# Optimization experiments

Measured on AMD Instinct MI355X. Metric: run time of the kernel, lower is better.

Reference implementation:

```python
import jax, jax.numpy as jnp
import numpy as np

EPS = 1e-5
HEADS = 8
DIM_HEAD = 64
SCALE = DIM_HEAD ** -0.5
DEPTH = 4


def _layernorm(x, g, b):
    mu = jnp.mean(x, axis=-1, keepdims=True)
    var = jnp.var(x, axis=-1, keepdims=True)
    return (x - mu) * jax.lax.rsqrt(var + EPS) * g + b


def setup_inputs() -> dict:
    key = jax.random.key(0)
    ks = jax.random.split(key, 8)
    b, n, dim, mlp = 4, 1024, 512, 2048
    inner = HEADS * DIM_HEAD
    D = DEPTH
    s = 0.02  # realistic init scale
    return {
        "x": jax.random.normal(ks[0], (b, n, dim), jnp.float32),
        "ln1_g": jnp.ones((D, dim), jnp.float32),
        "ln1_b": jnp.zeros((D, dim), jnp.float32),
        "w_qkv": jax.random.normal(ks[1], (D, dim, 3 * inner), jnp.float32) * s,
        "reattn_w": jax.random.normal(ks[2], (D, HEADS, HEADS), jnp.float32),
        "rln_g": jnp.ones((D, HEADS), jnp.float32),
        "rln_b": jnp.zeros((D, HEADS), jnp.float32),
        "w_out": jax.random.normal(ks[3], (D, inner, dim), jnp.float32) * s,
        "b_out": jnp.zeros((D, dim), jnp.float32),
        "ln2_g": jnp.ones((D, dim), jnp.float32),
        "ln2_b": jnp.zeros((D, dim), jnp.float32),
        "w1": jax.random.normal(ks[4], (D, dim, mlp), jnp.float32) * s,
        "b1": jnp.zeros((D, mlp), jnp.float32),
        "w2": jax.random.normal(ks[5], (D, mlp, dim), jnp.float32) * s,
        "b2": jnp.zeros((D, dim), jnp.float32),
    }


def _attention(x, ln_g, ln_b, w_qkv, rw, rg, rb, w_out, b_out):
    b, n, dim = x.shape
    h, d = HEADS, DIM_HEAD
    hn = _layernorm(x, ln_g, ln_b)
    qkv = hn @ w_qkv  # [b, n, 3*h*d]
    q, k, v = jnp.split(qkv, 3, axis=-1)
    def to_heads(t):
        return t.reshape(b, n, h, d).transpose(0, 2, 1, 3)  # b h n d
    q, k, v = to_heads(q), to_heads(k), to_heads(v)
    dots = jnp.einsum('bhid,bhjd->bhij', q, k) * SCALE
    attn = jax.nn.softmax(dots, axis=-1)
    # cross-head re-attention mix
    attn = jnp.einsum('bhij,hg->bgij', attn, rw)
    # LayerNorm over the head axis (axis=1)
    mu = jnp.mean(attn, axis=1, keepdims=True)
    var = jnp.var(attn, axis=1, keepdims=True)
    attn = (attn - mu) * jax.lax.rsqrt(var + EPS)
    attn = attn * rg[None, :, None, None] + rb[None, :, None, None]
    out = jnp.einsum('bhij,bhjd->bhid', attn, v)
    out = out.transpose(0, 2, 1, 3).reshape(b, n, h * d)
    return out @ w_out + b_out


def _ffn(x, ln_g, ln_b, w1, b1, w2, b2):
    hn = _layernorm(x, ln_g, ln_b)
    hid = jax.nn.gelu(hn @ w1 + b1, approximate=False)
    return hid @ w2 + b2


def reference(x, ln1_g, ln1_b, w_qkv, reattn_w, rln_g, rln_b, w_out, b_out,
              ln2_g, ln2_b, w1, b1, w2, b2):
    for l in range(DEPTH):
        x = x + _attention(x, ln1_g[l], ln1_b[l], w_qkv[l], reattn_w[l],
                           rln_g[l], rln_b[l], w_out[l], b_out[l])
        x = x + _ffn(x, ln2_g[l], ln2_b[l], w1[l], b1[l], w2[l], b2[l])
        x = jnp.tanh(x)
    return x
```

## Files before the change

kernel.cpp:

```cpp
#include <hip/hip_runtime.h>
#include <math.h>

#define B 4
#define N 1024
#define DM 512
#define H 8
#define MLP 2048
#define TOK (B * N)
#define QKVW (3 * DM)
#define EPS 1e-5f
#define SCALE 0.125f

#define PS_HN  ((long)TOK * DM)
#define PS_WQ  ((long)QKVW * DM)
#define PS_VT  ((long)B * H * 64 * N)

using short8 = __attribute__((ext_vector_type(8))) short;
using f32x4  = __attribute__((ext_vector_type(4))) float;
using u32x4  = __attribute__((ext_vector_type(4))) unsigned int;

__device__ __forceinline__ ushort f2b(float v) {
    unsigned int u = __builtin_bit_cast(unsigned int, v);
    u += 0x7fff + ((u >> 16) & 1);
    return (ushort)(u >> 16);
}
__device__ __forceinline__ float b2f(ushort u) {
    return __builtin_bit_cast(float, (unsigned int)u << 16);
}
__device__ __forceinline__ void split3(float v, ushort& h, ushort& l, ushort& q2) {
    h = f2b(v); float r1 = v - b2f(h);
    l = f2b(r1); q2 = f2b(r1 - b2f(l));
}
__device__ __forceinline__ void split_store8(f32x4 a0, f32x4 a1, char* base,
                                             int planeStride, int off) {
    short8 h8, l8, q8;
#pragma unroll
    for (int i = 0; i < 4; ++i) {
        ushort h, l, q;
        split3(a0[i], h, l, q);
        h8[i] = (short)h; l8[i] = (short)l; q8[i] = (short)q;
    }
#pragma unroll
    for (int i = 0; i < 4; ++i) {
        ushort h, l, q;
        split3(a1[i], h, l, q);
        h8[4 + i] = (short)h; l8[4 + i] = (short)l; q8[4 + i] = (short)q;
    }
    *(short8*)(base + off) = h8;
    *(short8*)(base + planeStride + off) = l8;
    *(short8*)(base + 2 * planeStride + off) = q8;
}

__global__ __launch_bounds__(256) void ln3_kernel(const float* __restrict__ x,
                                                  const float* __restrict__ g,
                                                  const float* __restrict__ bta,
                                                  ushort* __restrict__ out) {
    const int row = blockIdx.x;
    const int t = threadIdx.x;
    const float* xr = x + (size_t)row * DM;
    float v0 = xr[t], v1 = xr[t + 256];
    float s = v0 + v1, ss = v0 * v0 + v1 * v1;
    for (int o = 32; o; o >>= 1) {
        s += __shfl_down(s, o);
        ss += __shfl_down(ss, o);
    }
    __shared__ float ls[4], lss[4];
    const int wid = t >> 6, lane = t & 63;
    if (lane == 0) { ls[wid] = s; lss[wid] = ss; }
    __syncthreads();
    if (t == 0) {
        float S = ls[0] + ls[1] + ls[2] + ls[3];
        float SS = lss[0] + lss[1] + lss[2] + lss[3];
        float mu = S / DM;
        ls[0] = mu;
        lss[0] = SS / DM - mu * mu;
    }
    __syncthreads();
    const float mu = ls[0];
    const float r = rsqrtf(lss[0] + EPS);
    float o0 = (v0 - mu) * r * g[t] + bta[t];
    float o1 = (v1 - mu) * r * g[t + 256] + bta[t + 256];
    ushort h, l, q;
    size_t i0 = (size_t)row * DM + t;
    split3(o0, h, l, q);
    out[i0] = h; out[i0 + PS_HN] = l; out[i0 + 2 * PS_HN] = q;
    split3(o1, h, l, q);
    out[i0 + 256] = h; out[i0 + 256 + PS_HN] = l; out[i0 + 256 + 2 * PS_HN] = q;
}

__global__ __launch_bounds__(256) void wtrans_kernel(const float* __restrict__ W,
                                                     ushort* __restrict__ WT,
                                                     int K, int Nn, long ps) {
    __shared__ float ts[32][33];
    const int n0 = blockIdx.x * 32, k0 = blockIdx.y * 32;
    const int tx = threadIdx.x & 31, ty = threadIdx.x >> 5;
#pragma unroll
    for (int p = 0; p < 4; ++p)
        ts[ty + p * 8][tx] = W[(size_t)(k0 + ty + p * 8) * Nn + n0 + tx];
    __syncthreads();
#pragma unroll
    for (int p = 0; p < 4; ++p) {
        float v = ts[tx][ty + p * 8];
        ushort h, l, q;
        split3(v, h, l, q);
        size_t idx = (size_t)(n0 + ty + p * 8) * K + k0 + tx;
        WT[idx] = h;
        WT[idx + ps] = l;
        WT[idx + 2 * ps] = q;
    }
}

__global__ __launch_bounds__(256) void vtrans3_kernel(const float* __restrict__ v,
                                                      ushort* __restrict__ vt) {
    const int z = blockIdx.z, b = z >> 3, h = z & 7;
    __shared__ float ts[32][33];
    const int j0 = blockIdx.x * 32, d0 = blockIdx.y * 32;
    const int tx = threadIdx.x & 31, ty = threadIdx.x >> 5;
#pragma unroll
    for (int p = 0; p < 4; ++p)
        ts[ty + p * 8][tx] =
            v[(size_t)(b * N + j0 + ty + p * 8) * DM + h * 64 + d0 + tx];
    __syncthreads();
#pragma unroll
    for (int p = 0; p < 4; ++p) {
        float val = ts[tx][ty + p * 8];
        ushort hh, ll, qq;
        split3(val, hh, ll, qq);
        size_t dst = (size_t)((b * H + h) * 64 + d0 + ty + p * 8) * N + j0 + tx;
        vt[dst] = hh;
        vt[dst + PS_VT] = ll;
        vt[dst + 2 * PS_VT] = qq;
    }
}

template <int BM, int BN, int WR, int WC, int EPI, bool AF32, bool BF32, int KSPLIT>
__global__ __launch_bounds__(256) void mm3_kernel(
    const void* __restrict__ Av, int sA, long pA, long zA,
    const void* __restrict__ Bv, int sB, long pB, long zB,
    const float* __restrict__ bias, const float* __restrict__ res,
    void* __restrict__ Cv, int sC, long zC, int K, float scale) {
    constexpr int WM = BM / WR, WN = BN / WC;
    constexpr int FM = WM / 16, FN = WN / 16;
    constexpr int RA = BM / 64, RB = BN / 64;
    static_assert(!AF32 || RA == 1, "AF32 assumes BM==64");
    static_assert(!BF32 || RB <= 2, "BF32 assumes BN<=128");
    int bx, by, z;
    {
        const int gx = gridDim.x, gy = gridDim.y;
        const long nwg = (long)gx * gy * gridDim.z;
        long o = ((long)blockIdx.z * gy + blockIdx.y) * gx + blockIdx.x;
        if ((nwg & 7) == 0) { const long q = nwg >> 3; o = (o & 7) * q + (o >> 3); }
        bx = (int)(o % gx);
        const long r1 = o / gx;
        by = (int)(r1 % gy);
        z  = (int)(r1 / gy);
    }
    const ushort* A  = AF32 ? nullptr : (const ushort*)Av + (size_t)z * zA;
    const float*  Af = AF32 ? (const float*)Av + (size_t)z * zA : nullptr;
    const ushort* Bt = BF32 ? nullptr : (const ushort*)Bv + (size_t)z * zB;
    const float*  Bf = BF32 ? (const float*)Bv + (size_t)z * zB : nullptr;
    __shared__ char lds[3 * (BM + BN) * 64];
    char* Bbase = lds + 3 * BM * 64;
    const int t = threadIdx.x;
    const int lane = t & 63, w = t >> 6;
    const int wr = w / WC, wc = w % WC;
    const int m0 = by * BM, n0 = bx * BN;
    const int sr = t >> 2, skg = t & 3;
    const int off0 = sr * 64 + 16 * (skg ^ ((sr >> 1) & 3));

    f32x4 acc[FM][FN];
#pragma unroll
    for (int i = 0; i < FM; ++i)
#pragma unroll
        for (int j = 0; j < FN; ++j) acc[i][j] = (f32x4){0.f, 0.f, 0.f, 0.f};

    u32x4 cA[3][RA], nA[3][RA], cB[3][RB], nB[3][RB];
    f32x4 cAf[2], nAf[2], cBf[2 * RB], nBf[2 * RB];

    auto loadAll = [&](int KT, u32x4 (&DA)[3][RA], f32x4 (&DAf)[2],
                       u32x4 (&DB)[3][RB], f32x4 (&DBf)[2 * RB]) {
        if constexpr (AF32) {
            const float* s_ = Af + (size_t)(m0 + sr) * sA + KT + skg * 8;
            DAf[0] = *(const f32x4*)s_;
            DAf[1] = *(const f32x4*)(s_ + 4);
        } else {
#pragma unroll
            for (int pl = 0; pl < 3; ++pl)
#pragma unroll
                for (int p = 0; p < RA; ++p)
                    DA[pl][p] = *(const u32x4*)(A + (size_t)pl * pA +
                        (size_t)(m0 + sr + p * 64) * sA + KT + skg * 8);
        }
        if constexpr (BF32) {
#pragma unroll
            for (int p = 0; p < RB; ++p) {
                const float* s_ = Bf + (size_t)(n0 + sr + p * 64) * sB + KT + skg * 8;
                DBf[2 * p] = *(const f32x4*)s_;
                DBf[2 * p + 1] = *(const f32x4*)(s_ + 4);
            }
        } else {
#pragma unroll
            for (int pl = 0; pl < 3; ++pl)
#pragma unroll
                for (int p = 0; p < RB; ++p)
                    DB[pl][p] = *(const u32x4*)(Bt + (size_t)pl * pB +
                        (size_t)(n0 + sr + p * 64) * sB + KT + skg * 8);
        }
    };
    auto storeAll = [&](u32x4 (&DA)[3][RA], f32x4 (&DAf)[2],
                        u32x4 (&DB)[3][RB], f32x4 (&DBf)[2 * RB]) {
        if constexpr (AF32) {
            split_store8(DAf[0], DAf[1], lds, BM * 64, off0);
        } else {
#pragma unroll
            for (int pl = 0; pl < 3; ++pl)
#pragma unroll
                for (int p = 0; p < RA; ++p)
                    *(u32x4*)(lds + pl * BM * 64 + p * 4096 + off0) = DA[pl][p];
        }
        if constexpr (BF32) {
#pragma unroll
            for (int p = 0; p < RB; ++p)
                split_store8(DBf[2 * p], DBf[2 * p + 1], Bbase, BN * 64,
                             p * 4096 + off0);
        } else {
#pragma unroll
            for (int pl = 0; pl < 3; ++pl)
#pragma unroll
                for (int p = 0; p < RB; ++p)
                    *(u32x4*)(Bbase + pl * BN * 64 + p * 4096 + off0) = DB[pl][p];
        }
    };

    const int Kc = K / KSPLIT;
    const int kbeg = (KSPLIT > 1) ? z * Kc : 0;
    loadAll(kbeg, cA, cAf, cB, cBf);
    for (int kt = kbeg; kt < kbeg + Kc; kt += 32) {
        __syncthreads();
        storeAll(cA, cAf, cB, cBf);
        if (kt + 32 < kbeg + Kc) loadAll(kt + 32, nA, nAf, nB, nBf);
        __syncthreads();
        short8 af[3][FM], bf[3][FN];
        const int kg = lane >> 4;
#pragma unroll
        for (int pl = 0; pl < 3; ++pl)
#pragma unroll
            for (int i = 0; i < FM; ++i) {
                const int r = wr * WM + i * 16 + (lane & 15);
                af[pl][i] = *(const short8*)(lds + pl * BM * 64 + r * 64 +
                                             16 * (kg ^ ((r >> 1) & 3)));
            }
#pragma unroll
        for (int pl = 0; pl < 3; ++pl)
#pragma unroll
            for (int j = 0; j < FN; ++j) {
                const int r = wc * WN + j * 16 + (lane & 15);
                bf[pl][j] = *(const short8*)(Bbase + pl * BN * 64 + r * 64 +
                                             16 * (kg ^ ((r >> 1) & 3)));
            }
#pragma unroll
        for (int i = 0; i < FM; ++i)
#pragma unroll
            for (int j = 0; j < FN; ++j)
#pragma unroll
                for (int s = 2; s >= 0; --s)
#pragma unroll
                    for (int ph = 0; ph <= 2; ++ph) {
                        const int pb = s - ph;
                        if (pb < 0 || pb > 2) continue;
                        acc[i][j] = __builtin_amdgcn_mfma_f32_16x16x32_bf16(
                            af[ph][i], bf[pb][j], acc[i][j], 0, 0, 0);
                    }
        if constexpr (AF32) { cAf[0] = nAf[0]; cAf[1] = nAf[1]; }
        else {
#pragma unroll
            for (int pl = 0; pl < 3; ++pl)
#pragma unroll
                for (int p = 0; p < RA; ++p) cA[pl][p] = nA[pl][p];
        }
        if constexpr (BF32) {
#pragma unroll
            for (int p = 0; p < 2 * RB; ++p) cBf[p] = nBf[p];
        } else {
#pragma unroll
            for (int pl = 0; pl < 3; ++pl)
#pragma unroll
                for (int p = 0; p < RB; ++p) cB[pl][p] = nB[pl][p];
        }
    }
#pragma unroll
    for (int i = 0; i < FM; ++i) {
#pragma unroll
        for (int j = 0; j < FN; ++j) {
            const int col = n0 + wc * WN + j * 16 + (lane & 15);
#pragma unroll
            for (int r4 = 0; r4 < 4; ++r4) {
                const int row = m0 + wr * WM + i * 16 + (lane >> 4) * 4 + r4;
                float v = acc[i][j][r4];
                if (EPI == 1) v *= scale;
                if (EPI == 2) {
                    v += bias[col];
                    v = 0.5f * v * (1.0f + erff(v * 0.70710678118654752f));
                }
                if (EPI == 3) {
                    if (col < 1024)
                        ((float*)Cv)[(size_t)row * 1024 + col] = v;
                    else
                        const_cast<float*>(res)[(size_t)row * 512 + col - 1024] = v;
                } else {
                    ((float*)Cv + (size_t)z * zC)[(size_t)row * sC + col] = v;
                }
            }
        }
    }
}

template <bool TANH>
__global__ __launch_bounds__(256) void red2_kernel(const float* __restrict__ P,
                                                   const float* __restrict__ bias,
                                                   const float* __restrict__ X,
                                                   float* __restrict__ out) {
    const size_t e = ((size_t)blockIdx.x * 256 + threadIdx.x) * 4;
    f32x4 p0 = *(const f32x4*)(P + e);
    f32x4 p1 = *(const f32x4*)(P + (size_t)TOK * DM + e);
    f32x4 xb = *(const f32x4*)(X + e);
    f32x4 bb = *(const f32x4*)(bias + (e & (DM - 1)));
    f32x4 v;
#pragma unroll
    for (int i = 0; i < 4; ++i) {
        float r = xb[i] + p0[i] + p1[i] + bb[i];
        v[i] = TANH ? tanhf(r) : r;
    }
    *(f32x4*)(out + e) = v;
}

__global__ __launch_bounds__(256) void softmax_mix_kernel(float* __restrict__ d,
                                                          const float* __restrict__ rw,
                                                          const float* __restrict__ rg,
                                                          const float* __restrict__ rb) {
    const int i = blockIdx.x;
    const int t = threadIdx.x;
    const int lane = t & 63, wid = t >> 6;
    __shared__ float red[4];
    __shared__ float srw[64], srg[8], srb[8];
    if (t < 64) srw[t] = rw[t];
    if (t < 8) { srg[t] = rg[t]; srb[t] = rb[t]; }
    float p[8][4];
#pragma unroll
    for (int h = 0; h < 8; ++h) {
        const float* rowp = d + ((size_t)h * 1024 + i) * 1024;
        float lm = -1e30f;
#pragma unroll
        for (int u = 0; u < 4; ++u) {
            p[h][u] = rowp[t + u * 256];
            lm = fmaxf(lm, p[h][u]);
        }
        for (int o = 32; o; o >>= 1) lm = fmaxf(lm, __shfl_down(lm, o));
        __syncthreads();
        if (lane == 0) red[wid] = lm;
        __syncthreads();
        const float M = fmaxf(fmaxf(red[0], red[1]), fmaxf(red[2], red[3]));
        float ls = 0.f;
#pragma unroll
        for (int u = 0; u < 4; ++u) {
            p[h][u] = expf(p[h][u] - M);
            ls += p[h][u];
        }
        for (int o = 32; o; o >>= 1) ls += __shfl_down(ls, o);
        __syncthreads();
        if (lane == 0) red[wid] = ls;
        __syncthreads();
        const float inv = 1.0f / (red[0] + red[1] + red[2] + red[3]);
#pragma unroll
        for (int u = 0; u < 4; ++u) p[h][u] *= inv;
    }
#pragma unroll
    for (int u = 0; u < 4; ++u) {
        float mg[8];
#pragma unroll
        for (int g = 0; g < 8; ++g) {
            float acc = 0.f;
#pragma unroll
            for (int h = 0; h < 8; ++h) acc += p[h][u] * srw[h * 8 + g];
            mg[g] = acc;
        }
        float mean = 0.f;
#pragma unroll
        for (int g = 0; g < 8; ++g) mean += mg[g];
        mean *= 0.125f;
        float var = 0.f;
#pragma unroll
        for (int g = 0; g < 8; ++g) { float dd = mg[g] - mean; var += dd * dd; }
        var *= 0.125f;
        const float rs = rsqrtf(var + EPS);
#pragma unroll
        for (int g = 0; g < 8; ++g)
            d[((size_t)g * 1024 + i) * 1024 + t + u * 256] =
                (mg[g] - mean) * rs * srg[g] + srb[g];
    }
}

extern "C" void kernel_launch(void* const* d_in, const int* in_sizes, int n_in,
                              void* d_out, int out_size, void* d_ws, size_t ws_size,
                              hipStream_t stream) {
    const float* x_in  = (const float*)d_in[0];
    const float* ln1_g = (const float*)d_in[1];
    const float* ln1_b = (const float*)d_in[2];
    const float* w_qkv = (const float*)d_in[3];
    const float* re_w  = (const float*)d_in[4];
    const float* rln_g = (const float*)d_in[5];
    const float* rln_b = (const float*)d_in[6];
    const float* w_out = (const float*)d_in[7];
    const float* b_out = (const float*)d_in[8];
    const float* ln2_g = (const float*)d_in[9];
    const float* ln2_b = (const float*)d_in[10];
    const float* w1    = (const float*)d_in[11];
    const float* b1    = (const float*)d_in[12];
    const float* w2    = (const float*)d_in[13];
    const float* b2    = (const float*)d_in[14];

    char* wsb = (char*)d_ws;
    float*  X    = (float*)wsb;
    float*  QKf  = (float*)(wsb + (8ull << 20));
    ushort* VT3  = (ushort*)(wsb + (24ull << 20));
    float*  D    = (float*)(wsb + (36ull << 20));
    float*  AO   = (float*)(wsb + (68ull << 20));
    ushort* HN3  = (ushort*)(wsb + (36ull << 20));
    ushort* WQT  = (ushort*)(wsb + (48ull << 20));
    float*  Vf   = (float*)(wsb + (53ull << 20));
    ushort* WOT  = (ushort*)(wsb + (36ull << 20));
    float*  OPP  = (float*)(wsb + (38ull << 20));
    ushort* HN3f = (ushort*)(wsb + (8ull  << 20));
    ushort* W1T  = (ushort*)(wsb + (20ull << 20));
    ushort* W2T  = (ushort*)(wsb + (26ull << 20));
    float*  HIDf = (float*)(wsb + (36ull << 20));
    float*  FPP  = (float*)(wsb + (8ull  << 20));

    hipMemcpyAsync(X, x_in, sizeof(float) * (size_t)TOK * DM,
                   hipMemcpyDeviceToDevice, stream);

    for (int l = 0; l < 4; ++l) {
        ln3_kernel<<<TOK, 256, 0, stream>>>(X, ln1_g + l * DM, ln1_b + l * DM, HN3);
        wtrans_kernel<<<dim3(QKVW / 32, DM / 32), 256, 0, stream>>>(
            w_qkv + (size_t)l * DM * QKVW, WQT, DM, QKVW, PS_WQ);
        mm3_kernel<64, 128, 1, 4, 3, false, false, 1>
            <<<dim3(12, TOK / 64, 1), 256, 0, stream>>>(
            HN3, DM, PS_HN, 0, WQT, DM, PS_WQ, 0, nullptr, Vf,
            QKf, 1024, 0, DM, 1.f);
        vtrans3_kernel<<<dim3(N / 32, 2, B * H), 256, 0, stream>>>(Vf, VT3);

        for (int b = 0; b < B; ++b) {
            const float* qb = QKf + (size_t)b * N * 1024;
            mm3_kernel<64, 128, 1, 4, 1, true, true, 1>
                <<<dim3(8, 16, H), 256, 0, stream>>>(
                qb, 1024, 0, 64, qb + 512, 1024, 0, 64, nullptr, nullptr,
                D, 1024, (long)1024 * 1024, 64, SCALE);
            softmax_mix_kernel<<<N, 256, 0, stream>>>(
                D, re_w + l * H * H, rln_g + l * H, rln_b + l * H);
            mm3_kernel<64, 64, 2, 2, 0, true, false, 1>
                <<<dim3(1, 16, H), 256, 0, stream>>>(
                D, 1024, 0, (long)1024 * 1024,
                VT3 + (size_t)b * H * 64 * N, 1024, PS_VT, (long)64 * N,
                nullptr, nullptr,
                AO + (size_t)b * N * DM, DM, 64, N, 1.f);
        }
        wtrans_kernel<<<dim3(DM / 32, DM / 32), 256, 0, stream>>>(
            w_out + (size_t)l * DM * DM, WOT, DM, DM, (long)DM * DM);
        mm3_kernel<64, 128, 1, 4, 0, true, false, 2>
            <<<dim3(4, TOK / 64, 2), 256, 0, stream>>>(
            AO, DM, 0, 0, WOT, DM, (long)DM * DM, 0, nullptr, nullptr,
            OPP, DM, (long)TOK * DM, DM, 1.f);
        red2_kernel<false><<<TOK * DM / 1024, 256, 0, stream>>>(
            OPP, b_out + l * DM, X, X);

        ln3_kernel<<<TOK, 256, 0, stream>>>(X, ln2_g + l * DM, ln2_b + l * DM, HN3f);
        wtrans_kernel<<<dim3(MLP / 32, DM / 32), 256, 0, stream>>>(
            w1 + (size_t)l * DM * MLP, W1T, DM, MLP, (long)MLP * DM);
        mm3_kernel<64, 128, 1, 4, 2, false, false, 1>
            <<<dim3(MLP / 128, TOK / 64, 1), 256, 0, stream>>>(
            HN3f, DM, PS_HN, 0, W1T, DM, (long)MLP * DM, 0, b1 + l * MLP, nullptr,
            HIDf, MLP, 0, DM, 1.f);
        wtrans_kernel<<<dim3(DM / 32, MLP / 32), 256, 0, stream>>>(
            w2 + (size_t)l * MLP * DM, W2T, MLP, DM, (long)DM * MLP);
        mm3_kernel<64, 128, 1, 4, 0, true, false, 2>
            <<<dim3(4, TOK / 64, 2), 256, 0, stream>>>(
            HIDf, MLP, 0, 0, W2T, MLP, (long)DM * MLP, 0, nullptr, nullptr,
            FPP, DM, (long)TOK * DM, MLP, 1.f);
        float* outp = (l == 3) ? (float*)d_out : X;
        red2_kernel<true><<<TOK * DM / 1024, 256, 0, stream>>>(
            FPP, b2 + l * DM, X, outp);
    }
}
```

Before: 1.837 ms.

## Enlarge GEMM tiles, split-K attn·V with fp32 V, vectorize softmax-mix

Moves the QKV, QK^T, FFN1 and FFN2 GEMMs from 64x128 to 128x128 tiles with a 2x2 warp layout, and widens FFN2 split-K from 2 to 4. The attention·V GEMM now reads fp32 V directly, splitting it into three bf16 parts on the fly instead of pre-splitting it in the transpose. It also uses 4-way split-K with a new reduction kernel, to fill the GPU with more blocks. The softmax-mix kernel switches to vectorized f32x4 loads and stores. Together these aim to cut load traffic and raise occupancy, at the cost of extra partial-sum buffers, extra reduction launches and more registers per block.

New measurement: 1.739 ms. 1.06x faster.

```diff
diff --git a/kernel.cpp b/kernel.cpp
--- a/kernel.cpp
+++ b/kernel.cpp
@@ -13,7 +13,6 @@
 
 #define PS_HN  ((long)TOK * DM)
 #define PS_WQ  ((long)QKVW * DM)
-#define PS_VT  ((long)B * H * 64 * N)
 
 using short8 = __attribute__((ext_vector_type(8))) short;
 using f32x4  = __attribute__((ext_vector_type(4))) float;
@@ -110,8 +109,8 @@
     }
 }
 
-__global__ __launch_bounds__(256) void vtrans3_kernel(const float* __restrict__ v,
-                                                      ushort* __restrict__ vt) {
+__global__ __launch_bounds__(256) void vtrans_kernel(const float* __restrict__ v,
+                                                     float* __restrict__ vt) {
     const int z = blockIdx.z, b = z >> 3, h = z & 7;
     __shared__ float ts[32][33];
     const int j0 = blockIdx.x * 32, d0 = blockIdx.y * 32;
@@ -122,27 +121,21 @@
             v[(size_t)(b * N + j0 + ty + p * 8) * DM + h * 64 + d0 + tx];
     __syncthreads();
 #pragma unroll
-    for (int p = 0; p < 4; ++p) {
-        float val = ts[tx][ty + p * 8];
-        ushort hh, ll, qq;
-        split3(val, hh, ll, qq);
-        size_t dst = (size_t)((b * H + h) * 64 + d0 + ty + p * 8) * N + j0 + tx;
-        vt[dst] = hh;
-        vt[dst + PS_VT] = ll;
-        vt[dst + 2 * PS_VT] = qq;
-    }
-}
-
-template <int BM, int BN, int WR, int WC, int EPI, bool AF32, bool BF32, int KSPLIT>
+    for (int p = 0; p < 4; ++p)
+        vt[(size_t)((b * H + h) * 64 + d0 + ty + p * 8) * N + j0 + tx] =
+            ts[tx][ty + p * 8];
+}
+
+template <int BM, int BN, int WR, int WC, int EPI, bool AF32, bool BF32, int ZDIV>
 __global__ __launch_bounds__(256) void mm3_kernel(
     const void* __restrict__ Av, int sA, long pA, long zA,
     const void* __restrict__ Bv, int sB, long pB, long zB,
     const float* __restrict__ bias, const float* __restrict__ res,
-    void* __restrict__ Cv, int sC, long zC, int K, float scale) {
+    void* __restrict__ Cv, int sC, long zC, long zCk, int K, float scale) {
     constexpr int WM = BM / WR, WN = BN / WC;
     constexpr int FM = WM / 16, FN = WN / 16;
     constexpr int RA = BM / 64, RB = BN / 64;
-    static_assert(!AF32 || RA == 1, "AF32 assumes BM==64");
+    static_assert(!AF32 || RA <= 2, "AF32 assumes BM<=128");
     static_assert(!BF32 || RB <= 2, "BF32 assumes BN<=128");
     int bx, by, z;
     {
@@ -155,10 +148,11 @@
         by = (int)(r1 % gy);
         z  = (int)(r1 / gy);
     }
-    const ushort* A  = AF32 ? nullptr : (const ushort*)Av + (size_t)z * zA;
-    const float*  Af = AF32 ? (const float*)Av + (size_t)z * zA : nullptr;
-    const ushort* Bt = BF32 ? nullptr : (const ushort*)Bv + (size_t)z * zB;
-    const float*  Bf = BF32 ? (const float*)Bv + (size_t)z * zB : nullptr;
+    const int zo = z / ZDIV, zk = z % ZDIV;
+    const ushort* A  = AF32 ? nullptr : (const ushort*)Av + (size_t)zo * zA;
+    const float*  Af = AF32 ? (const float*)Av + (size_t)zo * zA : nullptr;
+    const ushort* Bt = BF32 ? nullptr : (const ushort*)Bv + (size_t)zo * zB;
+    const float*  Bf = BF32 ? (const float*)Bv + (size_t)zo * zB : nullptr;
     __shared__ char lds[3 * (BM + BN) * 64];
     char* Bbase = lds + 3 * BM * 64;
     const int t = threadIdx.x;
@@ -175,14 +169,17 @@
         for (int j = 0; j < FN; ++j) acc[i][j] = (f32x4){0.f, 0.f, 0.f, 0.f};
 
     u32x4 cA[3][RA], nA[3][RA], cB[3][RB], nB[3][RB];
-    f32x4 cAf[2], nAf[2], cBf[2 * RB], nBf[2 * RB];
-
-    auto loadAll = [&](int KT, u32x4 (&DA)[3][RA], f32x4 (&DAf)[2],
+    f32x4 cAf[2 * RA], nAf[2 * RA], cBf[2 * RB], nBf[2 * RB];
+
+    auto loadAll = [&](int KT, u32x4 (&DA)[3][RA], f32x4 (&DAf)[2 * RA],
                        u32x4 (&DB)[3][RB], f32x4 (&DBf)[2 * RB]) {
         if constexpr (AF32) {
-            const float* s_ = Af + (size_t)(m0 + sr) * sA + KT + skg * 8;
-            DAf[0] = *(const f32x4*)s_;
-            DAf[1] = *(const f32x4*)(s_ + 4);
+#pragma unroll
+            for (int p = 0; p < RA; ++p) {
+                const float* s_ = Af + (size_t)(m0 + sr + p * 64) * sA + KT + skg * 8;
+                DAf[2 * p] = *(const f32x4*)s_;
+                DAf[2 * p + 1] = *(const f32x4*)(s_ + 4);
+            }
         } else {
 #pragma unroll
             for (int pl = 0; pl < 3; ++pl)
@@ -207,10 +204,13 @@
                         (size_t)(n0 + sr + p * 64) * sB + KT + skg * 8);
         }
     };
-    auto storeAll = [&](u32x4 (&DA)[3][RA], f32x4 (&DAf)[2],
+    auto storeAll = [&](u32x4 (&DA)[3][RA], f32x4 (&DAf)[2 * RA],
                         u32x4 (&DB)[3][RB], f32x4 (&DBf)[2 * RB]) {
         if constexpr (AF32) {
-            split_store8(DAf[0], DAf[1], lds, BM * 64, off0);
+#pragma unroll
+            for (int p = 0; p < RA; ++p)
+                split_store8(DAf[2 * p], DAf[2 * p + 1], lds, BM * 64,
+                             p * 4096 + off0);
         } else {
 #pragma unroll
             for (int pl = 0; pl < 3; ++pl)
@@ -232,8 +232,8 @@
         }
     };
 
-    const int Kc = K / KSPLIT;
-    const int kbeg = (KSPLIT > 1) ? z * Kc : 0;
+    const int Kc = K / ZDIV;
+    const int kbeg = zk * Kc;
     loadAll(kbeg, cA, cAf, cB, cBf);
     for (int kt = kbeg; kt < kbeg + Kc; kt += 32) {
         __syncthreads();
@@ -271,8 +271,10 @@
                         acc[i][j] = __builtin_amdgcn_mfma_f32_16x16x32_bf16(
                             af[ph][i], bf[pb][j], acc[i][j], 0, 0, 0);
                     }
-        if constexpr (AF32) { cAf[0] = nAf[0]; cAf[1] = nAf[1]; }
-        else {
+        if constexpr (AF32) {
+#pragma unroll
+            for (int p = 0; p < 2 * RA; ++p) cAf[p] = nAf[p];
+        } else {
 #pragma unroll
             for (int pl = 0; pl < 3; ++pl)
 #pragma unroll
@@ -288,6 +290,7 @@
                 for (int p = 0; p < RB; ++p) cB[pl][p] = nB[pl][p];
         }
     }
+    float* Cbase = (float*)Cv + (size_t)zo * zC + (size_t)zk * zCk;
 #pragma unroll
     for (int i = 0; i < FM; ++i) {
 #pragma unroll
@@ -308,30 +311,37 @@
                     else
                         const_cast<float*>(res)[(size_t)row * 512 + col - 1024] = v;
                 } else {
-                    ((float*)Cv + (size_t)z * zC)[(size_t)row * sC + col] = v;
+                    Cbase[(size_t)row * sC + col] = v;
                 }
             }
         }
     }
 }
 
-template <bool TANH>
-__global__ __launch_bounds__(256) void red2_kernel(const float* __restrict__ P,
-                                                   const float* __restrict__ bias,
-                                                   const float* __restrict__ X,
-                                                   float* __restrict__ out) {
+template <int KS, int MODE>
+__global__ __launch_bounds__(256) void red_kernel(const float* __restrict__ P,
+                                                  long pstride,
+                                                  const float* __restrict__ bias,
+                                                  const float* __restrict__ X,
+                                                  float* __restrict__ out) {
     const size_t e = ((size_t)blockIdx.x * 256 + threadIdx.x) * 4;
-    f32x4 p0 = *(const f32x4*)(P + e);
-    f32x4 p1 = *(const f32x4*)(P + (size_t)TOK * DM + e);
-    f32x4 xb = *(const f32x4*)(X + e);
-    f32x4 bb = *(const f32x4*)(bias + (e & (DM - 1)));
-    f32x4 v;
-#pragma unroll
-    for (int i = 0; i < 4; ++i) {
-        float r = xb[i] + p0[i] + p1[i] + bb[i];
-        v[i] = TANH ? tanhf(r) : r;
-    }
-    *(f32x4*)(out + e) = v;
+    f32x4 a = *(const f32x4*)(P + e);
+#pragma unroll
+    for (int k = 1; k < KS; ++k) {
+        f32x4 pk = *(const f32x4*)(P + (size_t)k * pstride + e);
+#pragma unroll
+        for (int i = 0; i < 4; ++i) a[i] += pk[i];
+    }
+    if (MODE >= 1) {
+        f32x4 xb = *(const f32x4*)(X + e);
+        f32x4 bb = *(const f32x4*)(bias + (e & (DM - 1)));
+#pragma unroll
+        for (int i = 0; i < 4; ++i) {
+            float r = xb[i] + a[i] + bb[i];
+            a[i] = (MODE == 2) ? tanhf(r) : r;
+        }
+    }
+    *(f32x4*)(out + e) = a;
 }
 
 __global__ __launch_bounds__(256) void softmax_mix_kernel(float* __restrict__ d,
@@ -345,16 +355,11 @@
     __shared__ float srw[64], srg[8], srb[8];
     if (t < 64) srw[t] = rw[t];
     if (t < 8) { srg[t] = rg[t]; srb[t] = rb[t]; }
-    float p[8][4];
+    f32x4 p[8];
 #pragma unroll
     for (int h = 0; h < 8; ++h) {
-        const float* rowp = d + ((size_t)h * 1024 + i) * 1024;
-        float lm = -1e30f;
-#pragma unroll
-        for (int u = 0; u < 4; ++u) {
-            p[h][u] = rowp[t + u * 256];
-            lm = fmaxf(lm, p[h][u]);
-        }
+        p[h] = ((const f32x4*)(d + ((size_t)h * 1024 + i) * 1024))[t];
+        float lm = fmaxf(fmaxf(p[h][0], p[h][1]), fmaxf(p[h][2], p[h][3]));
         for (int o = 32; o; o >>= 1) lm = fmaxf(lm, __shfl_down(lm, o));
         __syncthreads();
         if (lane == 0) red[wid] = lm;
@@ -374,30 +379,34 @@
 #pragma unroll
         for (int u = 0; u < 4; ++u) p[h][u] *= inv;
     }
+    f32x4 mg[8];
+#pragma unroll
+    for (int g = 0; g < 8; ++g) {
+#pragma unroll
+        for (int u = 0; u < 4; ++u) {
+            float acc = 0.f;
+#pragma unroll
+            for (int h = 0; h < 8; ++h) acc += p[h][u] * srw[h * 8 + g];
+            mg[g][u] = acc;
+        }
+    }
 #pragma unroll
     for (int u = 0; u < 4; ++u) {
-        float mg[8];
-#pragma unroll
-        for (int g = 0; g < 8; ++g) {
-            float acc = 0.f;
-#pragma unroll
-            for (int h = 0; h < 8; ++h) acc += p[h][u] * srw[h * 8 + g];
-            mg[g] = acc;
-        }
         float mean = 0.f;
 #pragma unroll
-        for (int g = 0; g < 8; ++g) mean += mg[g];
+        for (int g = 0; g < 8; ++g) mean += mg[g][u];
         mean *= 0.125f;
         float var = 0.f;
 #pragma unroll
-        for (int g = 0; g < 8; ++g) { float dd = mg[g] - mean; var += dd * dd; }
+        for (int g = 0; g < 8; ++g) { float dd = mg[g][u] - mean; var += dd * dd; }
         var *= 0.125f;
         const float rs = rsqrtf(var + EPS);
 #pragma unroll
-        for (int g = 0; g < 8; ++g)
-            d[((size_t)g * 1024 + i) * 1024 + t + u * 256] =
-                (mg[g] - mean) * rs * srg[g] + srb[g];
-    }
+        for (int g = 0; g < 8; ++g) mg[g][u] = (mg[g][u] - mean) * rs * srg[g] + srb[g];
+    }
+#pragma unroll
+    for (int g = 0; g < 8; ++g)
+        ((f32x4*)(d + ((size_t)g * 1024 + i) * 1024))[t] = mg[g];
 }
 
 extern "C" void kernel_launch(void* const* d_in, const int* in_sizes, int n_in,
@@ -422,18 +431,19 @@
     char* wsb = (char*)d_ws;
     float*  X    = (float*)wsb;
     float*  QKf  = (float*)(wsb + (8ull << 20));
-    ushort* VT3  = (ushort*)(wsb + (24ull << 20));
-    float*  D    = (float*)(wsb + (36ull << 20));
-    float*  AO   = (float*)(wsb + (68ull << 20));
-    ushort* HN3  = (ushort*)(wsb + (36ull << 20));
-    ushort* WQT  = (ushort*)(wsb + (48ull << 20));
-    float*  Vf   = (float*)(wsb + (53ull << 20));
-    ushort* WOT  = (ushort*)(wsb + (36ull << 20));
-    float*  OPP  = (float*)(wsb + (38ull << 20));
+    float*  VTf  = (float*)(wsb + (24ull << 20));
+    float*  D    = (float*)(wsb + (32ull << 20));
+    float*  AO   = (float*)(wsb + (64ull << 20));
+    float*  PVP  = (float*)(wsb + (72ull << 20));
+    ushort* HN3  = (ushort*)(wsb + (32ull << 20));
+    ushort* WQT  = (ushort*)(wsb + (44ull << 20));
+    float*  Vf   = (float*)(wsb + (49ull << 20));
+    ushort* WOT  = (ushort*)(wsb + (32ull << 20));
+    float*  OPP  = (float*)(wsb + (34ull << 20));
     ushort* HN3f = (ushort*)(wsb + (8ull  << 20));
     ushort* W1T  = (ushort*)(wsb + (20ull << 20));
-    ushort* W2T  = (ushort*)(wsb + (26ull << 20));
-    float*  HIDf = (float*)(wsb + (36ull << 20));
+    ushort* W2T  = (ushort*)(wsb + (40ull << 20));
+    float*  HIDf = (float*)(wsb + (48ull << 20));
     float*  FPP  = (float*)(wsb + (8ull  << 20));
 
     hipMemcpyAsync(X, x_in, sizeof(float) * (size_t)TOK * DM,
@@ -443,51 +453,53 @@
         ln3_kernel<<<TOK, 256, 0, stream>>>(X, ln1_g + l * DM, ln1_b + l * DM, HN3);
         wtrans_kernel<<<dim3(QKVW / 32, DM / 32), 256, 0, stream>>>(
             w_qkv + (size_t)l * DM * QKVW, WQT, DM, QKVW, PS_WQ);
-        mm3_kernel<64, 128, 1, 4, 3, false, false, 1>
-            <<<dim3(12, TOK / 64, 1), 256, 0, stream>>>(
+        mm3_kernel<128, 128, 2, 2, 3, false, false, 1>
+            <<<dim3(12, TOK / 128, 1), 256, 0, stream>>>(
             HN3, DM, PS_HN, 0, WQT, DM, PS_WQ, 0, nullptr, Vf,
-            QKf, 1024, 0, DM, 1.f);
-        vtrans3_kernel<<<dim3(N / 32, 2, B * H), 256, 0, stream>>>(Vf, VT3);
+            QKf, 1024, 0, 0, DM, 1.f);
+        vtrans_kernel<<<dim3(N / 32, 2, B * H), 256, 0, stream>>>(Vf, VTf);
 
         for (int b = 0; b < B; ++b) {
             const float* qb = QKf + (size_t)b * N * 1024;
-            mm3_kernel<64, 128, 1, 4, 1, true, true, 1>
-                <<<dim3(8, 16, H), 256, 0, stream>>>(
+            mm3_kernel<128, 128, 2, 2, 1, true, true, 1>
+                <<<dim3(8, 8, H), 256, 0, stream>>>(
                 qb, 1024, 0, 64, qb + 512, 1024, 0, 64, nullptr, nullptr,
-                D, 1024, (long)1024 * 1024, 64, SCALE);
+                D, 1024, (long)1024 * 1024, 0, 64, SCALE);
             softmax_mix_kernel<<<N, 256, 0, stream>>>(
                 D, re_w + l * H * H, rln_g + l * H, rln_b + l * H);
-            mm3_kernel<64, 64, 2, 2, 0, true, false, 1>
-                <<<dim3(1, 16, H), 256, 0, stream>>>(
+            mm3_kernel<64, 64, 2, 2, 0, true, true, 4>
+                <<<dim3(1, 16, H * 4), 256, 0, stream>>>(
                 D, 1024, 0, (long)1024 * 1024,
-                VT3 + (size_t)b * H * 64 * N, 1024, PS_VT, (long)64 * N,
+                VTf + (size_t)b * H * 64 * N, 1024, 0, (long)64 * N,
                 nullptr, nullptr,
-                AO + (size_t)b * N * DM, DM, 64, N, 1.f);
+                PVP, DM, 64, (long)N * DM, N, 1.f);
+            red_kernel<4, 0><<<N * DM / 1024, 256, 0, stream>>>(
+                PVP, (long)N * DM, nullptr, nullptr, AO + (size_t)b * N * DM);
         }
         wtrans_kernel<<<dim3(DM / 32, DM / 32), 256, 0, stream>>>(
             w_out + (size_t)l * DM * DM, WOT, DM, DM, (long)DM * DM);
         mm3_kernel<64, 128, 1, 4, 0, true, false, 2>
             <<<dim3(4, TOK / 64, 2), 256, 0, stream>>>(
             AO, DM, 0, 0, WOT, DM, (long)DM * DM, 0, nullptr, nullptr,
-            OPP, DM, (long)TOK * DM, DM, 1.f);
-        red2_kernel<false><<<TOK * DM / 1024, 256, 0, stream>>>(
-            OPP, b_out + l * DM, X, X);
+            OPP, DM, 0, (long)TOK * DM, DM, 1.f);
+        red_kernel<2, 1><<<TOK * DM / 1024, 256, 0, stream>>>(
+            OPP, (long)TOK * DM, b_out + l * DM, X, X);
 
         ln3_kernel<<<TOK, 256, 0, stream>>>(X, ln2_g + l * DM, ln2_b + l * DM, HN3f);
         wtrans_kernel<<<dim3(MLP / 32, DM / 32), 256, 0, stream>>>(
             w1 + (size_t)l * DM * MLP, W1T, DM, MLP, (long)MLP * DM);
-        mm3_kernel<64, 128, 1, 4, 2, false, false, 1>
-            <<<dim3(MLP / 128, TOK / 64, 1), 256, 0, stream>>>(
+        mm3_kernel<128, 128, 2, 2, 2, false, false, 1>
+            <<<dim3(MLP / 128, TOK / 128, 1), 256, 0, stream>>>(
             HN3f, DM, PS_HN, 0, W1T, DM, (long)MLP * DM, 0, b1 + l * MLP, nullptr,
-            HIDf, MLP, 0, DM, 1.f);
+            HIDf, MLP, 0, 0, DM, 1.f);
         wtrans_kernel<<<dim3(DM / 32, MLP / 32), 256, 0, stream>>>(
             w2 + (size_t)l * MLP * DM, W2T, MLP, DM, (long)DM * MLP);
-        mm3_kernel<64, 128, 1, 4, 0, true, false, 2>
-            <<<dim3(4, TOK / 64, 2), 256, 0, stream>>>(
+        mm3_kernel<128, 128, 2, 2, 0, true, false, 4>
+            <<<dim3(4, TOK / 128, 4), 256, 0, stream>>>(
             HIDf, MLP, 0, 0, W2T, MLP, (long)DM * MLP, 0, nullptr, nullptr,
-            FPP, DM, (long)TOK * DM, MLP, 1.f);
+            FPP, DM, 0, (long)TOK * DM, MLP, 1.f);
         float* outp = (l == 3) ? (float*)d_out : X;
-        red2_kernel<true><<<TOK * DM / 1024, 256, 0, stream>>>(
-            FPP, b2 + l * DM, X, outp);
-    }
-}
+        red_kernel<4, 2><<<TOK * DM / 1024, 256, 0, stream>>>(
+            FPP, (long)TOK * DM, b2 + l * DM, X, outp);
+    }
+}
```
